# Optimization experiments

Hardware: AMD Instinct MI355X
Metric: run time of the kernel (lower is better)

The kernel has to match this reference:

```python
import jax, jax.numpy as jnp
import numpy as np

N = 4096
IN_F = 256
OUT_F = 128
K = 3
BETA = 0.5
ALPHA = 0.2  # leaky relu negative slope
NEG_BIG = -9e15


def setup_inputs() -> dict:
    key = jax.random.key(0)
    k1, k2, k3, k4 = jax.random.split(key, 4)
    h = jax.random.normal(k1, (N, IN_F), dtype=jnp.float32)
    k_mask_list = jax.random.randint(k2, (K, N, N), 0, 2, dtype=jnp.int32)
    # xavier_uniform with gain=1.414
    def xavier(k, shape, gain=1.414):
        fan_in, fan_out = shape[0], shape[1]
        bound = gain * np.sqrt(6.0 / (fan_in + fan_out))
        return jax.random.uniform(k, shape, jnp.float32, -bound, bound)
    W = xavier(k3, (IN_F * K, OUT_F))
    a = xavier(k4, (2 * OUT_F * K, 1))
    return {"h": h, "k_mask_list": k_mask_list, "W": W, "a": a}


def reference(h, k_mask_list, W, a):
    # dropout p=0.0 / eval mode -> identity
    Wh = None
    for i in range(K - 1, -1, -1):
        Whnew = h @ W[i * IN_F:(i + 1) * IN_F, :]              # [N, OUT_F]
        if i == K - 1:
            Wh = Whnew
        a1 = a[2 * i * OUT_F:(2 * i + 1) * OUT_F, :]           # [OUT_F, 1]
        a2 = a[(2 * i + 1) * OUT_F:(2 * i + 2) * OUT_F, :]     # [OUT_F, 1]
        Wh1 = Whnew @ a1                                        # [N, 1]
        Wh2 = Whnew @ a2                                        # [N, 1]
        e = jax.nn.leaky_relu(Wh1 + Wh2.T, negative_slope=ALPHA)  # [N, N]
        masked = jnp.where(k_mask_list[i] > 0, e, NEG_BIG)
        attention = jax.nn.softmax(masked, axis=1)              # [N, N]
        Wh = (1.0 - BETA) * (attention @ Whnew) + BETA * Wh
    return jax.nn.elu(Wh)  # concat=True
```

## Files before the change

### kernel.cpp

```cpp
#include <hip/hip_runtime.h>
#include <hip/hip_bf16.h>

#define NN 4096
#define IN_F 256
#define OUT_F 128
#define ALPHA 0.2f

typedef __bf16 bf16x8 __attribute__((ext_vector_type(8)));
typedef float f32x4 __attribute__((ext_vector_type(4)));

__device__ __forceinline__ unsigned short f2bf(float f) {
  union { float f; unsigned int u; } x; x.f = f;
  unsigned int r = x.u + 0x7FFF + ((x.u >> 16) & 1);
  return (unsigned short)(r >> 16);
}

__global__ __launch_bounds__(256) void k_cvt_h(const float* __restrict__ h,
                                               unsigned short* __restrict__ hb) {
  int idx = (blockIdx.x * 256 + threadIdx.x) * 8;
  float4 v0 = *(const float4*)(h + idx);
  float4 v1 = *(const float4*)(h + idx + 4);
  union { unsigned short u[8]; uint4 q; } o;
  o.u[0] = f2bf(v0.x); o.u[1] = f2bf(v0.y); o.u[2] = f2bf(v0.z); o.u[3] = f2bf(v0.w);
  o.u[4] = f2bf(v1.x); o.u[5] = f2bf(v1.y); o.u[6] = f2bf(v1.z); o.u[7] = f2bf(v1.w);
  *(uint4*)(hb + idx) = o.q;
}

__global__ __launch_bounds__(256) void k_cvt_w(const float* __restrict__ W,
                                               unsigned short* __restrict__ Wtb) {
  const int i = blockIdx.y;
  const int k0 = blockIdx.x * 32;
  const int t = threadIdx.x;
  __shared__ float tile[32][129];
  #pragma unroll
  for (int j = 0; j < 16; ++j) {
    int idx = t + j * 256;
    int r = idx >> 7, c = idx & 127;
    tile[r][c] = W[(size_t)(i * IN_F + k0 + r) * OUT_F + c];
  }
  __syncthreads();
  const int c = t >> 1, half = t & 1;
  unsigned short* dst = Wtb + ((size_t)i * OUT_F + c) * IN_F + k0 + half * 16;
  #pragma unroll
  for (int g = 0; g < 4; ++g) {
    ushort4 v;
    v.x = f2bf(tile[half * 16 + g * 4 + 0][c]);
    v.y = f2bf(tile[half * 16 + g * 4 + 1][c]);
    v.z = f2bf(tile[half * 16 + g * 4 + 2][c]);
    v.w = f2bf(tile[half * 16 + g * 4 + 3][c]);
    *(ushort4*)(dst + g * 4) = v;
  }
}

__global__ __launch_bounds__(256) void k_zero(float* __restrict__ p) {
  int idx = blockIdx.x * 256 + threadIdx.x;
  f32x4 z = {0.f, 0.f, 0.f, 0.f};
  *(f32x4*)(p + (size_t)idx * 4) = z;
}

__global__ __launch_bounds__(256) void k_front(const unsigned short* __restrict__ hb,
                                               const unsigned short* __restrict__ Wtb,
                                               const float* __restrict__ a,
                                               float* __restrict__ Whnew2,
                                               unsigned short* __restrict__ Vt,
                                               float* __restrict__ Wh1,
                                               float* __restrict__ Wh2) {
  const int i = blockIdx.y;
  const int r0 = blockIdx.x * 32;
  const int t = threadIdx.x;
  const int lane = t & 63, wid = t >> 6;
  const int m = wid & 1, nh = wid >> 1, nbase = nh * 64;
  const int ln = lane & 15, lk = lane >> 4;

  __shared__ float a1s[128], a2s[128];
  __shared__ unsigned short tT[128][34];
  __shared__ float red1[2][32], red2[2][32];

  if (t < 128) {
    a1s[t] = a[(size_t)2 * i * OUT_F + t];
    a2s[t] = a[(size_t)(2 * i + 1) * OUT_F + t];
  }
  __syncthreads();

  const unsigned short* ap = hb + (size_t)(r0 + m * 16 + ln) * IN_F + lk * 8;
  const unsigned short* bp = Wtb + ((size_t)i * OUT_F + nbase + ln) * IN_F + lk * 8;

  f32x4 z4 = {0.f, 0.f, 0.f, 0.f};
  f32x4 acc[4] = {z4, z4, z4, z4};
  #pragma unroll
  for (int ks = 0; ks < 8; ++ks) {
    bf16x8 av = *(const bf16x8*)(ap + ks * 32);
    acc[0] = __builtin_amdgcn_mfma_f32_16x16x32_bf16(av, *(const bf16x8*)(bp + 0 * 16 * IN_F + ks * 32), acc[0], 0, 0, 0);
    acc[1] = __builtin_amdgcn_mfma_f32_16x16x32_bf16(av, *(const bf16x8*)(bp + 1 * 16 * IN_F + ks * 32), acc[1], 0, 0, 0);
    acc[2] = __builtin_amdgcn_mfma_f32_16x16x32_bf16(av, *(const bf16x8*)(bp + 2 * 16 * IN_F + ks * 32), acc[2], 0, 0, 0);
    acc[3] = __builtin_amdgcn_mfma_f32_16x16x32_bf16(av, *(const bf16x8*)(bp + 3 * 16 * IN_F + ks * 32), acc[3], 0, 0, 0);
  }

  float d1[4] = {0.f, 0.f, 0.f, 0.f}, d2[4] = {0.f, 0.f, 0.f, 0.f};
  #pragma unroll
  for (int f = 0; f < 4; ++f) {
    const int col = nbase + f * 16 + ln;
    const float va1 = a1s[col], va2 = a2s[col];
    #pragma unroll
    for (int q = 0; q < 4; ++q) {
      const int row = m * 16 + lk * 4 + q;
      const float v = acc[f][q];
      if (i == 2) Whnew2[(size_t)(r0 + row) * OUT_F + col] = v;
      tT[col][row] = f2bf(v);
      d1[q] += v * va1;
      d2[q] += v * va2;
    }
  }
  #pragma unroll
  for (int msk = 1; msk < 16; msk <<= 1) {
    #pragma unroll
    for (int q = 0; q < 4; ++q) {
      d1[q] += __shfl_xor(d1[q], msk, 64);
      d2[q] += __shfl_xor(d2[q], msk, 64);
    }
  }
  if (ln == 0) {
    #pragma unroll
    for (int q = 0; q < 4; ++q) {
      red1[nh][m * 16 + lk * 4 + q] = d1[q];
      red2[nh][m * 16 + lk * 4 + q] = d2[q];
    }
  }
  __syncthreads();

  if (t < 32) {
    Wh1[(size_t)i * NN + r0 + t] = red1[0][t] + red1[1][t];
    Wh2[(size_t)i * NN + r0 + t] = red2[0][t] + red2[1][t];
  }
  {
    const int c = t >> 1, half = t & 1;
    unsigned short* dst = Vt + ((size_t)i * OUT_F + c) * NN + r0 + half * 16;
    union { unsigned short u[8]; uint4 q; } o0, o1;
    #pragma unroll
    for (int j = 0; j < 8; ++j) { o0.u[j] = tT[c][half * 16 + j]; o1.u[j] = tT[c][half * 16 + 8 + j]; }
    *(uint4*)(dst) = o0.q;
    *(uint4*)(dst + 8) = o1.q;
  }
}

__global__ __launch_bounds__(256) void k_gmax(const float* __restrict__ Wh2,
                                              float* __restrict__ gmax2) {
  const int i = blockIdx.x;
  const int t = threadIdx.x;
  __shared__ float red[4];
  float m = -3.0e38f;
  #pragma unroll
  for (int j = 0; j < 16; ++j) m = fmaxf(m, Wh2[(size_t)i * NN + t + j * 256]);
  #pragma unroll
  for (int o = 32; o > 0; o >>= 1) m = fmaxf(m, __shfl_down(m, o, 64));
  if ((t & 63) == 0) red[t >> 6] = m;
  __syncthreads();
  if (t == 0) gmax2[i] = fmaxf(fmaxf(red[0], red[1]), fmaxf(red[2], red[3]));
}

__global__ __launch_bounds__(256) void k_attn(const unsigned short* __restrict__ Vt,
                                              const int* __restrict__ mask,
                                              const float* __restrict__ Wh1,
                                              const float* __restrict__ Wh2,
                                              const float* __restrict__ gmax2,
                                              float* __restrict__ U,
                                              float* __restrict__ S) {
  const int i = blockIdx.y;
  const int r0 = blockIdx.x * 32;
  const int c0 = blockIdx.z * (NN / 4);
  const int t = threadIdx.x;
  const int lane = t & 63, wid = t >> 6;
  const int m = wid & 1, nh = wid >> 1, nbase = nh * 64;
  const int ln = lane & 15, lk = lane >> 4;

  __shared__ unsigned short P[2][32 * 128];
  __shared__ float wh1s[32], mxs[32];

  if (t < 32) {
    float w1 = Wh1[(size_t)i * NN + r0 + t];
    wh1s[t] = w1;
    float e = w1 + gmax2[i];
    mxs[t] = (e > 0.f) ? e : ALPHA * e;
  }
  __syncthreads();

  const int* mbase = mask + ((size_t)i * NN + r0) * NN + c0;
  const float* wh2 = Wh2 + (size_t)i * NN + c0;

  const unsigned short* bp0 = Vt + ((size_t)i * OUT_F + nbase +  0 + ln) * NN + c0 + lk * 8;
  const unsigned short* bp1 = Vt + ((size_t)i * OUT_F + nbase + 16 + ln) * NN + c0 + lk * 8;
  const unsigned short* bp2 = Vt + ((size_t)i * OUT_F + nbase + 32 + ln) * NN + c0 + lk * 8;
  const unsigned short* bp3 = Vt + ((size_t)i * OUT_F + nbase + 48 + ln) * NN + c0 + lk * 8;

  const int arow = m * 16 + ln;
  const int abase = arow * 256;
  const int axor = (arow & 7) << 4;

  f32x4 z4 = {0.f, 0.f, 0.f, 0.f};
  f32x4 acc0 = z4, acc1 = z4, acc2 = z4, acc3 = z4, accS = z4;
  bf16x8 ones = {(__bf16)1.0f, (__bf16)1.0f, (__bf16)1.0f, (__bf16)1.0f,
                 (__bf16)1.0f, (__bf16)1.0f, (__bf16)1.0f, (__bf16)1.0f};

  int4 mk[4];
  float4 w2[4];

  auto LOADM = [&](int c) {
    const int k0 = c * 128;
    #pragma unroll
    for (int j = 0; j < 4; ++j) {
      int idx = t * 4 + j * 1024;
      int r = idx >> 7, dc = idx & 127;
      mk[j] = *(const int4*)(mbase + (size_t)r * NN + k0 + dc);
      w2[j] = *(const float4*)(wh2 + k0 + dc);
    }
  };
  auto COMP = [&](int buf) {
    #pragma unroll
    for (int j = 0; j < 4; ++j) {
      int idx = t * 4 + j * 1024;
      int r = idx >> 7, dc = idx & 127;
      float w1 = wh1s[r], mx = mxs[r];
      float e0 = w1 + w2[j].x; e0 = (e0 > 0.f) ? e0 : ALPHA * e0;
      float e1 = w1 + w2[j].y; e1 = (e1 > 0.f) ? e1 : ALPHA * e1;
      float e2 = w1 + w2[j].z; e2 = (e2 > 0.f) ? e2 : ALPHA * e2;
      float e3 = w1 + w2[j].w; e3 = (e3 > 0.f) ? e3 : ALPHA * e3;
      ushort4 pv;
      pv.x = (mk[j].x > 0) ? f2bf(__expf(e0 - mx)) : 0;
      pv.y = (mk[j].y > 0) ? f2bf(__expf(e1 - mx)) : 0;
      pv.z = (mk[j].z > 0) ? f2bf(__expf(e2 - mx)) : 0;
      pv.w = (mk[j].w > 0) ? f2bf(__expf(e3 - mx)) : 0;
      *(ushort4*)((char*)&P[buf][0] + ((r * 256 + dc * 2) ^ ((r & 7) << 4))) = pv;
    }
  };

  LOADM(0);
  COMP(0);
  __syncthreads();
  LOADM(1);

  for (int c = 0; c < 8; ++c) {
    const int cur = c & 1;
    const int k0 = c * 128;
    #pragma unroll
    for (int ks = 0; ks < 4; ++ks) {
      bf16x8 av = *(const bf16x8*)((const char*)&P[cur][0]
                                   + ((abase + lk * 16 + ks * 64) ^ axor));
      const int koff = k0 + ks * 32;
      acc0 = __builtin_amdgcn_mfma_f32_16x16x32_bf16(av, *(const bf16x8*)(bp0 + koff), acc0, 0, 0, 0);
      acc1 = __builtin_amdgcn_mfma_f32_16x16x32_bf16(av, *(const bf16x8*)(bp1 + koff), acc1, 0, 0, 0);
      acc2 = __builtin_amdgcn_mfma_f32_16x16x32_bf16(av, *(const bf16x8*)(bp2 + koff), acc2, 0, 0, 0);
      acc3 = __builtin_amdgcn_mfma_f32_16x16x32_bf16(av, *(const bf16x8*)(bp3 + koff), acc3, 0, 0, 0);
      if (nh == 0) accS = __builtin_amdgcn_mfma_f32_16x16x32_bf16(av, ones, accS, 0, 0, 0);
    }
    if (c < 7) COMP(cur ^ 1);
    __syncthreads();
    if (c < 6) LOADM(c + 2);
  }

  if (nh == 0 && ln == 0) {
    #pragma unroll
    for (int q = 0; q < 4; ++q)
      atomicAdd(&S[(size_t)i * NN + r0 + m * 16 + lk * 4 + q], accS[q]);
  }
  #pragma unroll
  for (int q = 0; q < 4; ++q) {
    const int row = m * 16 + lk * 4 + q;
    float* urow = U + ((size_t)i * NN + r0 + row) * OUT_F + nbase + ln;
    atomicAdd(urow +  0, acc0[q]);
    atomicAdd(urow + 16, acc1[q]);
    atomicAdd(urow + 32, acc2[q]);
    atomicAdd(urow + 48, acc3[q]);
  }
}

__global__ __launch_bounds__(256) void k_final(const float* __restrict__ U,
                                               const float* __restrict__ S,
                                               const float* __restrict__ Whnew2,
                                               float* __restrict__ out) {
  int idx = blockIdx.x * 256 + threadIdx.x;
  int r = idx >> 7;
  float v = 0.5f   * U[idx] / S[r]
          + 0.25f  * U[(size_t)NN * OUT_F + idx] / S[NN + r]
          + 0.125f * U[(size_t)2 * NN * OUT_F + idx] / S[2 * NN + r]
          + 0.125f * Whnew2[idx];
  out[idx] = (v > 0.f) ? v : (expf(v) - 1.0f);
}

extern "C" void kernel_launch(void* const* d_in, const int* in_sizes, int n_in,
                              void* d_out, int out_size, void* d_ws, size_t ws_size,
                              hipStream_t stream) {
  const float* h    = (const float*)d_in[0];
  const int*   mask = (const int*)d_in[1];
  const float* W    = (const float*)d_in[2];
  const float* a    = (const float*)d_in[3];
  float* out = (float*)d_out;

  float* Whnew2 = (float*)d_ws;
  float* Wh1    = Whnew2 + (size_t)NN * OUT_F;
  float* Wh2    = Wh1 + 3 * NN;
  float* gmax2  = Wh2 + 3 * NN;
  float* U      = gmax2 + 4;
  float* S      = U + (size_t)3 * NN * OUT_F;
  unsigned short* hb  = (unsigned short*)(S + 3 * NN);
  unsigned short* Wtb = hb + (size_t)NN * IN_F;
  unsigned short* Vt  = Wtb + (size_t)3 * OUT_F * IN_F;

  k_cvt_h<<<512, 256, 0, stream>>>(h, hb);
  k_cvt_w<<<dim3(8, 3), 256, 0, stream>>>(W, Wtb);
  k_zero<<<(3 * NN * OUT_F + 3 * NN) / 1024, 256, 0, stream>>>(U);
  k_front<<<dim3(128, 3), 256, 0, stream>>>(hb, Wtb, a, Whnew2, Vt, Wh1, Wh2);
  k_gmax<<<3, 256, 0, stream>>>(Wh2, gmax2);
  k_attn<<<dim3(128, 3, 4), 256, 0, stream>>>(Vt, mask, Wh1, Wh2, gmax2, U, S);
  k_final<<<(NN * OUT_F) / 256, 256, 0, stream>>>(U, S, Whnew2, out);
}
```

Before: 400.7 us.

## Factor leaky-relu exponentials into rank-1 terms and bit-pack mask for attention matmul

The attention weights exp(leaky(w1+w2)-mx) are split by the sign of w1+w2 into exp(w1)·exp(w2) or exp(αw1)·exp(αw2). The column factors are folded into two pre-scaled bf16 copies of Whnew, and the mask plus sign condition is packed into bitmasks in a separate pass that also computes the row sums. The attention kernel then expands the bits into 0/1 bf16 operands and runs 32x32 MFMAs over both scaled value matrices, applying the row factors at the end. This removes the per-element exp work from the inner loop and cuts mask traffic to a single int32 read. In exchange the MFMA work doubles, there are more kernels and intermediate buffers, and large unnormalized exponentials in bf16 could lose precision or overflow.

```diff
diff --git a/kernel.cpp b/kernel.cpp
--- a/kernel.cpp
+++ b/kernel.cpp
@@ -8,11 +8,25 @@
 
 typedef __bf16 bf16x8 __attribute__((ext_vector_type(8)));
 typedef float f32x4 __attribute__((ext_vector_type(4)));
-
+typedef float f32x16 __attribute__((ext_vector_type(16)));
+
+__device__ __forceinline__ float bf2f(unsigned short u) {
+  return __uint_as_float(((unsigned int)u) << 16);
+}
 __device__ __forceinline__ unsigned short f2bf(float f) {
   union { float f; unsigned int u; } x; x.f = f;
   unsigned int r = x.u + 0x7FFF + ((x.u >> 16) & 1);
   return (unsigned short)(r >> 16);
+}
+__device__ __forceinline__ bf16x8 bits2bf8(unsigned int b) {
+  union { unsigned int u[4]; bf16x8 v; } o;
+  #pragma unroll
+  for (int e = 0; e < 4; ++e) {
+    unsigned int lo = (b >> (2 * e)) & 1u;
+    unsigned int hi = (b >> (2 * e + 1)) & 1u;
+    o.u[e] = lo * 0x3F80u + hi * 0x3F800000u;
+  }
+  return o.v;
 }
 
 __global__ __launch_bounds__(256) void k_cvt_h(const float* __restrict__ h,
@@ -61,8 +75,7 @@
 __global__ __launch_bounds__(256) void k_front(const unsigned short* __restrict__ hb,
                                                const unsigned short* __restrict__ Wtb,
                                                const float* __restrict__ a,
-                                               float* __restrict__ Whnew2,
-                                               unsigned short* __restrict__ Vt,
+                                               float* __restrict__ Whnewf,
                                                float* __restrict__ Wh1,
                                                float* __restrict__ Wh2) {
   const int i = blockIdx.y;
@@ -73,7 +86,6 @@
   const int ln = lane & 15, lk = lane >> 4;
 
   __shared__ float a1s[128], a2s[128];
-  __shared__ unsigned short tT[128][34];
   __shared__ float red1[2][32], red2[2][32];
 
   if (t < 128) {
@@ -105,8 +117,7 @@
     for (int q = 0; q < 4; ++q) {
       const int row = m * 16 + lk * 4 + q;
       const float v = acc[f][q];
-      if (i == 2) Whnew2[(size_t)(r0 + row) * OUT_F + col] = v;
-      tT[col][row] = f2bf(v);
+      Whnewf[((size_t)i * NN + r0 + row) * OUT_F + col] = v;
       d1[q] += v * va1;
       d2[q] += v * va2;
     }
@@ -127,20 +138,10 @@
     }
   }
   __syncthreads();
-
   if (t < 32) {
     Wh1[(size_t)i * NN + r0 + t] = red1[0][t] + red1[1][t];
     Wh2[(size_t)i * NN + r0 + t] = red2[0][t] + red2[1][t];
   }
-  {
-    const int c = t >> 1, half = t & 1;
-    unsigned short* dst = Vt + ((size_t)i * OUT_F + c) * NN + r0 + half * 16;
-    union { unsigned short u[8]; uint4 q; } o0, o1;
-    #pragma unroll
-    for (int j = 0; j < 8; ++j) { o0.u[j] = tT[c][half * 16 + j]; o1.u[j] = tT[c][half * 16 + 8 + j]; }
-    *(uint4*)(dst) = o0.q;
-    *(uint4*)(dst + 8) = o1.q;
-  }
 }
 
 __global__ __launch_bounds__(256) void k_gmax(const float* __restrict__ Wh2,
@@ -158,132 +159,226 @@
   if (t == 0) gmax2[i] = fmaxf(fmaxf(red[0], red[1]), fmaxf(red[2], red[3]));
 }
 
-__global__ __launch_bounds__(256) void k_attn(const unsigned short* __restrict__ Vt,
-                                              const int* __restrict__ mask,
+__global__ __launch_bounds__(256) void k_ew2(const float* __restrict__ Wh2,
+                                             unsigned short* __restrict__ ew2pb,
+                                             unsigned short* __restrict__ ew2mb) {
+  int id = blockIdx.x * 256 + threadIdx.x;
+  float w2 = Wh2[id];
+  ew2pb[id] = f2bf(__expf(w2));
+  ew2mb[id] = f2bf(__expf(ALPHA * w2));
+}
+
+__global__ __launch_bounds__(256) void k_scale(const float* __restrict__ Whnewf,
+                                               const unsigned short* __restrict__ ew2pb,
+                                               const unsigned short* __restrict__ ew2mb,
+                                               unsigned short* __restrict__ Vkm) {
+  const int i = blockIdx.y;
+  const int k0 = blockIdx.x * 32;
+  const int t = threadIdx.x;
+  __shared__ float tile[32][129];
+  __shared__ float ewsp[32], ewsm[32];
+  if (t < 32) {
+    ewsp[t] = bf2f(ew2pb[(size_t)i * NN + k0 + t]);
+    ewsm[t] = bf2f(ew2mb[(size_t)i * NN + k0 + t]);
+  }
+  #pragma unroll
+  for (int j = 0; j < 16; ++j) {
+    int idx = t + j * 256;
+    int r = idx >> 7, c = idx & 127;
+    tile[r][c] = Whnewf[((size_t)i * NN + k0 + r) * OUT_F + c];
+  }
+  __syncthreads();
+  const int n = t >> 1, half = t & 1;
+  unsigned short* dstP = Vkm + ((size_t)(i * 2 + 0) * OUT_F + n) * NN + k0 + half * 16;
+  unsigned short* dstM = Vkm + ((size_t)(i * 2 + 1) * OUT_F + n) * NN + k0 + half * 16;
+  #pragma unroll
+  for (int g = 0; g < 4; ++g) {
+    ushort4 vp, vm;
+    float x0 = tile[half * 16 + g * 4 + 0][n];
+    float x1 = tile[half * 16 + g * 4 + 1][n];
+    float x2 = tile[half * 16 + g * 4 + 2][n];
+    float x3 = tile[half * 16 + g * 4 + 3][n];
+    vp.x = f2bf(ewsp[half * 16 + g * 4 + 0] * x0);
+    vp.y = f2bf(ewsp[half * 16 + g * 4 + 1] * x1);
+    vp.z = f2bf(ewsp[half * 16 + g * 4 + 2] * x2);
+    vp.w = f2bf(ewsp[half * 16 + g * 4 + 3] * x3);
+    vm.x = f2bf(ewsm[half * 16 + g * 4 + 0] * x0);
+    vm.y = f2bf(ewsm[half * 16 + g * 4 + 1] * x1);
+    vm.z = f2bf(ewsm[half * 16 + g * 4 + 2] * x2);
+    vm.w = f2bf(ewsm[half * 16 + g * 4 + 3] * x3);
+    *(ushort4*)(dstP + g * 4) = vp;
+    *(ushort4*)(dstM + g * 4) = vm;
+  }
+}
+
+__global__ __launch_bounds__(256) void k_bits(const int* __restrict__ mask,
                                               const float* __restrict__ Wh1,
                                               const float* __restrict__ Wh2,
-                                              const float* __restrict__ gmax2,
-                                              float* __restrict__ U,
-                                              float* __restrict__ S) {
+                                              const unsigned short* __restrict__ ew2pb,
+                                              const unsigned short* __restrict__ ew2mb,
+                                              unsigned int* __restrict__ Bits,
+                                              float* __restrict__ Sp,
+                                              float* __restrict__ Sm) {
   const int i = blockIdx.y;
-  const int r0 = blockIdx.x * 32;
-  const int c0 = blockIdx.z * (NN / 4);
+  const int r0 = blockIdx.x * 8;
+  const int t = threadIdx.x;
+  const int lane = t & 63, wid = t >> 6;
+  __shared__ float partP[8][4], partM[8][4];
+  float w2v[16], ep[16], em[16];
+  #pragma unroll
+  for (int j = 0; j < 16; ++j) {
+    int c = t * 16 + j;
+    w2v[j] = Wh2[(size_t)i * NN + c];
+    ep[j] = bf2f(ew2pb[(size_t)i * NN + c]);
+    em[j] = bf2f(ew2mb[(size_t)i * NN + c]);
+  }
+  const int* mbase = mask + ((size_t)i * NN + r0) * NN + t * 16;
+  int mA[16], mB[16];
+  auto LD = [&](int rr, int* mv) {
+    #pragma unroll
+    for (int jj = 0; jj < 4; ++jj) {
+      int4 v = *(const int4*)(mbase + (size_t)rr * NN + jj * 4);
+      mv[jj * 4 + 0] = v.x; mv[jj * 4 + 1] = v.y;
+      mv[jj * 4 + 2] = v.z; mv[jj * 4 + 3] = v.w;
+    }
+  };
+  auto PR = [&](int rr, const int* mv) {
+    const int r = r0 + rr;
+    const float nw1 = -Wh1[(size_t)i * NN + r];
+    unsigned int bp = 0, bm = 0;
+    float sp = 0.f, sm = 0.f;
+    #pragma unroll
+    for (int j = 0; j < 16; ++j) {
+      bool mm = mv[j] > 0;
+      bool cc = w2v[j] > nw1;
+      if (mm && cc)  { bp |= 1u << j; sp += ep[j]; }
+      if (mm && !cc) { bm |= 1u << j; sm += em[j]; }
+    }
+    Bits[((size_t)i * NN + r) * 256 + t] = bp | (bm << 16);
+    #pragma unroll
+    for (int o = 1; o < 64; o <<= 1) {
+      sp += __shfl_xor(sp, o, 64);
+      sm += __shfl_xor(sm, o, 64);
+    }
+    if (lane == 0) { partP[rr][wid] = sp; partM[rr][wid] = sm; }
+  };
+  LD(0, mA);
+  #pragma unroll
+  for (int rp = 0; rp < 4; ++rp) {
+    LD(2 * rp + 1, mB);
+    PR(2 * rp, mA);
+    if (rp < 3) LD(2 * rp + 2, mA);
+    PR(2 * rp + 1, mB);
+  }
+  __syncthreads();
+  if (t < 8) {
+    Sp[(size_t)i * NN + r0 + t] = partP[t][0] + partP[t][1] + partP[t][2] + partP[t][3];
+    Sm[(size_t)i * NN + r0 + t] = partM[t][0] + partM[t][1] + partM[t][2] + partM[t][3];
+  }
+}
+
+__global__ __launch_bounds__(256) void k_attn2(const unsigned short* __restrict__ Vkm,
+                                               const unsigned int* __restrict__ Bits,
+                                               const float* __restrict__ Wh1,
+                                               const float* __restrict__ gmax2,
+                                               float* __restrict__ U) {
+  const int i = blockIdx.y;
+  const int r0 = blockIdx.x * 64;
+  const int cb = blockIdx.z * 1024;
   const int t = threadIdx.x;
   const int lane = t & 63, wid = t >> 6;
   const int m = wid & 1, nh = wid >> 1, nbase = nh * 64;
-  const int ln = lane & 15, lk = lane >> 4;
-
-  __shared__ unsigned short P[2][32 * 128];
-  __shared__ float wh1s[32], mxs[32];
-
-  if (t < 32) {
-    float w1 = Wh1[(size_t)i * NN + r0 + t];
-    wh1s[t] = w1;
-    float e = w1 + gmax2[i];
-    mxs[t] = (e > 0.f) ? e : ALPHA * e;
-  }
-  __syncthreads();
-
-  const int* mbase = mask + ((size_t)i * NN + r0) * NN + c0;
-  const float* wh2 = Wh2 + (size_t)i * NN + c0;
-
-  const unsigned short* bp0 = Vt + ((size_t)i * OUT_F + nbase +  0 + ln) * NN + c0 + lk * 8;
-  const unsigned short* bp1 = Vt + ((size_t)i * OUT_F + nbase + 16 + ln) * NN + c0 + lk * 8;
-  const unsigned short* bp2 = Vt + ((size_t)i * OUT_F + nbase + 32 + ln) * NN + c0 + lk * 8;
-  const unsigned short* bp3 = Vt + ((size_t)i * OUT_F + nbase + 48 + ln) * NN + c0 + lk * 8;
-
-  const int arow = m * 16 + ln;
-  const int abase = arow * 256;
-  const int axor = (arow & 7) << 4;
-
-  f32x4 z4 = {0.f, 0.f, 0.f, 0.f};
-  f32x4 acc0 = z4, acc1 = z4, acc2 = z4, acc3 = z4, accS = z4;
-  bf16x8 ones = {(__bf16)1.0f, (__bf16)1.0f, (__bf16)1.0f, (__bf16)1.0f,
-                 (__bf16)1.0f, (__bf16)1.0f, (__bf16)1.0f, (__bf16)1.0f};
-
-  int4 mk[4];
-  float4 w2[4];
-
-  auto LOADM = [&](int c) {
-    const int k0 = c * 128;
-    #pragma unroll
-    for (int j = 0; j < 4; ++j) {
-      int idx = t * 4 + j * 1024;
-      int r = idx >> 7, dc = idx & 127;
-      mk[j] = *(const int4*)(mbase + (size_t)r * NN + k0 + dc);
-      w2[j] = *(const float4*)(wh2 + k0 + dc);
-    }
-  };
-  auto COMP = [&](int buf) {
-    #pragma unroll
-    for (int j = 0; j < 4; ++j) {
-      int idx = t * 4 + j * 1024;
-      int r = idx >> 7, dc = idx & 127;
-      float w1 = wh1s[r], mx = mxs[r];
-      float e0 = w1 + w2[j].x; e0 = (e0 > 0.f) ? e0 : ALPHA * e0;
-      float e1 = w1 + w2[j].y; e1 = (e1 > 0.f) ? e1 : ALPHA * e1;
-      float e2 = w1 + w2[j].z; e2 = (e2 > 0.f) ? e2 : ALPHA * e2;
-      float e3 = w1 + w2[j].w; e3 = (e3 > 0.f) ? e3 : ALPHA * e3;
-      ushort4 pv;
-      pv.x = (mk[j].x > 0) ? f2bf(__expf(e0 - mx)) : 0;
-      pv.y = (mk[j].y > 0) ? f2bf(__expf(e1 - mx)) : 0;
-      pv.z = (mk[j].z > 0) ? f2bf(__expf(e2 - mx)) : 0;
-      pv.w = (mk[j].w > 0) ? f2bf(__expf(e3 - mx)) : 0;
-      *(ushort4*)((char*)&P[buf][0] + ((r * 256 + dc * 2) ^ ((r & 7) << 4))) = pv;
-    }
-  };
-
-  LOADM(0);
-  COMP(0);
-  __syncthreads();
-  LOADM(1);
-
-  for (int c = 0; c < 8; ++c) {
-    const int cur = c & 1;
-    const int k0 = c * 128;
-    #pragma unroll
-    for (int ks = 0; ks < 4; ++ks) {
-      bf16x8 av = *(const bf16x8*)((const char*)&P[cur][0]
-                                   + ((abase + lk * 16 + ks * 64) ^ axor));
-      const int koff = k0 + ks * 32;
-      acc0 = __builtin_amdgcn_mfma_f32_16x16x32_bf16(av, *(const bf16x8*)(bp0 + koff), acc0, 0, 0, 0);
-      acc1 = __builtin_amdgcn_mfma_f32_16x16x32_bf16(av, *(const bf16x8*)(bp1 + koff), acc1, 0, 0, 0);
-      acc2 = __builtin_amdgcn_mfma_f32_16x16x32_bf16(av, *(const bf16x8*)(bp2 + koff), acc2, 0, 0, 0);
-      acc3 = __builtin_amdgcn_mfma_f32_16x16x32_bf16(av, *(const bf16x8*)(bp3 + koff), acc3, 0, 0, 0);
-      if (nh == 0) accS = __builtin_amdgcn_mfma_f32_16x16x32_bf16(av, ones, accS, 0, 0, 0);
-    }
-    if (c < 7) COMP(cur ^ 1);
+  const int l31 = lane & 31, kh = lane >> 5;
+
+  __shared__ char Vl[32768];
+  __shared__ float wh1s[64];
+
+  if (t < 64) wh1s[t] = Wh1[(size_t)i * NN + r0 + t];
+
+  const int r = r0 + m * 32 + l31;
+  const unsigned int* brow = Bits + ((size_t)i * NN + r) * 256 + (cb >> 4);
+
+  f32x16 accP0 = {}, accP1 = {}, accM0 = {}, accM1 = {};
+
+  for (int chunk = 0; chunk < 16; ++chunk) {
+    uint4 stg[8];
+    #pragma unroll
+    for (int j = 0; j < 8; ++j) {
+      int idx = t + j * 256;
+      int s = idx >> 10, n = (idx >> 3) & 127, g = idx & 7;
+      stg[j] = *(const uint4*)(Vkm + ((size_t)(i * 2 + s) * OUT_F + n) * NN + cb + chunk * 64 + g * 8);
+    }
+    const uint4 wv4 = *(const uint4*)(brow + chunk * 4);
+    unsigned int wv[4] = {wv4.x, wv4.y, wv4.z, wv4.w};
+
     __syncthreads();
-    if (c < 6) LOADM(c + 2);
-  }
-
-  if (nh == 0 && ln == 0) {
-    #pragma unroll
-    for (int q = 0; q < 4; ++q)
-      atomicAdd(&S[(size_t)i * NN + r0 + m * 16 + lk * 4 + q], accS[q]);
-  }
-  #pragma unroll
-  for (int q = 0; q < 4; ++q) {
-    const int row = m * 16 + lk * 4 + q;
-    float* urow = U + ((size_t)i * NN + r0 + row) * OUT_F + nbase + ln;
-    atomicAdd(urow +  0, acc0[q]);
-    atomicAdd(urow + 16, acc1[q]);
-    atomicAdd(urow + 32, acc2[q]);
-    atomicAdd(urow + 48, acc3[q]);
+    #pragma unroll
+    for (int j = 0; j < 8; ++j) {
+      int idx = t + j * 256;
+      int s = idx >> 10, n = (idx >> 3) & 127, g = idx & 7;
+      *(uint4*)(Vl + ((s << 14) + (n << 7) + (((g ^ (n & 7)) & 7) << 4))) = stg[j];
+    }
+    __syncthreads();
+
+    #pragma unroll
+    for (int kst = 0; kst < 4; ++kst) {
+      unsigned int bP = (wv[kst] >> (kh * 8)) & 0xFFu;
+      unsigned int bM = (wv[kst] >> (16 + kh * 8)) & 0xFFu;
+      bf16x8 aP = bits2bf8(bP);
+      bf16x8 aM = bits2bf8(bM);
+      const int slot = kst * 2 + kh;
+      const int n0 = nbase + l31;
+      const int n1 = nbase + 32 + l31;
+      bf16x8 bP0 = *(const bf16x8*)(Vl + ((0 << 14) + (n0 << 7) + (((slot ^ (n0 & 7)) & 7) << 4)));
+      bf16x8 bP1 = *(const bf16x8*)(Vl + ((0 << 14) + (n1 << 7) + (((slot ^ (n1 & 7)) & 7) << 4)));
+      bf16x8 bM0 = *(const bf16x8*)(Vl + ((1 << 14) + (n0 << 7) + (((slot ^ (n0 & 7)) & 7) << 4)));
+      bf16x8 bM1 = *(const bf16x8*)(Vl + ((1 << 14) + (n1 << 7) + (((slot ^ (n1 & 7)) & 7) << 4)));
+      accP0 = __builtin_amdgcn_mfma_f32_32x32x16_bf16(aP, bP0, accP0, 0, 0, 0);
+      accP1 = __builtin_amdgcn_mfma_f32_32x32x16_bf16(aP, bP1, accP1, 0, 0, 0);
+      accM0 = __builtin_amdgcn_mfma_f32_32x32x16_bf16(aM, bM0, accM0, 0, 0, 0);
+      accM1 = __builtin_amdgcn_mfma_f32_32x32x16_bf16(aM, bM1, accM1, 0, 0, 0);
+    }
+  }
+
+  const float gi = gmax2[i];
+  #pragma unroll
+  for (int q = 0; q < 16; ++q) {
+    const int crow = (q & 3) + 8 * (q >> 2) + 4 * kh;
+    const int rloc2 = m * 32 + crow;
+    const float w1 = wh1s[rloc2];
+    const float e0 = w1 + gi;
+    const float mx = (e0 > 0.f) ? e0 : ALPHA * e0;
+    const float fp = __expf(w1 - mx);
+    const float fm = __expf(ALPHA * w1 - mx);
+    float* urow = U + ((size_t)i * NN + r0 + rloc2) * OUT_F + nbase + l31;
+    atomicAdd(urow, fp * accP0[q] + fm * accM0[q]);
+    atomicAdd(urow + 32, fp * accP1[q] + fm * accM1[q]);
   }
 }
 
 __global__ __launch_bounds__(256) void k_final(const float* __restrict__ U,
-                                               const float* __restrict__ S,
-                                               const float* __restrict__ Whnew2,
+                                               const float* __restrict__ Sp,
+                                               const float* __restrict__ Sm,
+                                               const float* __restrict__ Wh1,
+                                               const float* __restrict__ gmax2,
+                                               const float* __restrict__ Whnewf,
                                                float* __restrict__ out) {
   int idx = blockIdx.x * 256 + threadIdx.x;
   int r = idx >> 7;
-  float v = 0.5f   * U[idx] / S[r]
-          + 0.25f  * U[(size_t)NN * OUT_F + idx] / S[NN + r]
-          + 0.125f * U[(size_t)2 * NN * OUT_F + idx] / S[2 * NN + r]
-          + 0.125f * Whnew2[idx];
-  out[idx] = (v > 0.f) ? v : (expf(v) - 1.0f);
+  float v = 0.125f * Whnewf[(size_t)2 * NN * OUT_F + idx];
+  #pragma unroll
+  for (int i = 0; i < 3; ++i) {
+    const float coef = (i == 0) ? 0.5f : (i == 1) ? 0.25f : 0.125f;
+    const float w1 = Wh1[(size_t)i * NN + r];
+    const float gi = gmax2[i];
+    const float e0 = w1 + gi;
+    const float mx = (e0 > 0.f) ? e0 : ALPHA * e0;
+    const float fp = __expf(w1 - mx);
+    const float fm = __expf(ALPHA * w1 - mx);
+    const float S = fp * Sp[(size_t)i * NN + r] + fm * Sm[(size_t)i * NN + r];
+    v += coef * U[(size_t)i * NN * OUT_F + idx] / S;
+  }
+  out[idx] = (v > 0.f) ? v : (__expf(v) - 1.0f);
 }
 
 extern "C" void kernel_launch(void* const* d_in, const int* in_sizes, int n_in,
@@ -295,21 +390,28 @@
   const float* a    = (const float*)d_in[3];
   float* out = (float*)d_out;
 
-  float* Whnew2 = (float*)d_ws;
-  float* Wh1    = Whnew2 + (size_t)NN * OUT_F;
+  float* Whnewf = (float*)d_ws;
+  float* Wh1    = Whnewf + (size_t)3 * NN * OUT_F;
   float* Wh2    = Wh1 + 3 * NN;
   float* gmax2  = Wh2 + 3 * NN;
   float* U      = gmax2 + 4;
-  float* S      = U + (size_t)3 * NN * OUT_F;
-  unsigned short* hb  = (unsigned short*)(S + 3 * NN);
-  unsigned short* Wtb = hb + (size_t)NN * IN_F;
-  unsigned short* Vt  = Wtb + (size_t)3 * OUT_F * IN_F;
+  float* Sp     = U + (size_t)3 * NN * OUT_F;
+  float* Sm     = Sp + 3 * NN;
+  unsigned short* hb    = (unsigned short*)(Sm + 3 * NN);
+  unsigned short* Wtb   = hb + (size_t)NN * IN_F;
+  unsigned short* Vkm   = Wtb + (size_t)3 * OUT_F * IN_F;
+  unsigned short* ew2pb = Vkm + (size_t)3 * 2 * OUT_F * NN;
+  unsigned short* ew2mb = ew2pb + 3 * NN;
+  unsigned int*   Bits  = (unsigned int*)(ew2mb + 3 * NN);
 
   k_cvt_h<<<512, 256, 0, stream>>>(h, hb);
   k_cvt_w<<<dim3(8, 3), 256, 0, stream>>>(W, Wtb);
-  k_zero<<<(3 * NN * OUT_F + 3 * NN) / 1024, 256, 0, stream>>>(U);
-  k_front<<<dim3(128, 3), 256, 0, stream>>>(hb, Wtb, a, Whnew2, Vt, Wh1, Wh2);
+  k_zero<<<(3 * NN * OUT_F) / 1024, 256, 0, stream>>>(U);
+  k_front<<<dim3(128, 3), 256, 0, stream>>>(hb, Wtb, a, Whnewf, Wh1, Wh2);
   k_gmax<<<3, 256, 0, stream>>>(Wh2, gmax2);
-  k_attn<<<dim3(128, 3, 4), 256, 0, stream>>>(Vt, mask, Wh1, Wh2, gmax2, U, S);
-  k_final<<<(NN * OUT_F) / 256, 256, 0, stream>>>(U, S, Whnew2, out);
-}
+  k_ew2<<<48, 256, 0, stream>>>(Wh2, ew2pb, ew2mb);
+  k_scale<<<dim3(128, 3), 256, 0, stream>>>(Whnewf, ew2pb, ew2mb, Vkm);
+  k_bits<<<dim3(512, 3), 256, 0, stream>>>(mask, Wh1, Wh2, ew2pb, ew2mb, Bits, Sp, Sm);
+  k_attn2<<<dim3(64, 3, 4), 256, 0, stream>>>(Vkm, Bits, Wh1, gmax2, U);
+  k_final<<<(NN * OUT_F) / 256, 256, 0, stream>>>(U, Sp, Sm, Wh1, gmax2, Whnewf, out);
+}
```

Result: slower. 465.2 us (+16.1%).
